# Optimization experiments

Hardware: AMD Instinct MI355X
Metric: run time of the kernel (lower is better)

## Reference

```python
import jax, jax.numpy as jnp
import numpy as np

B, L, E = 4, 2048, 1024
H, DQ, DV = 8, 128, 128
SCALE = 1.0 / np.sqrt(DQ).astype(np.float32)


def setup_inputs() -> dict:
    key = jax.random.key(0)
    ks = jax.random.split(key, 6)
    return {
        "qInputs": jax.random.normal(ks[0], (B, L, E), dtype=jnp.float32),
        "kvInputs": jax.random.normal(ks[1], (B, L, E), dtype=jnp.float32),
        "mask": jnp.zeros((B, H, L, L), dtype=jnp.bool_),
        "W_Q": jax.random.normal(ks[2], (E, H * DQ), dtype=jnp.float32) * 0.02,
        "W_K": jax.random.normal(ks[3], (E, H * DQ), dtype=jnp.float32) * 0.02,
        "W_V": jax.random.normal(ks[4], (E, H * DV), dtype=jnp.float32) * 0.02,
        "W_fc": jax.random.normal(ks[5], (H * DV, E), dtype=jnp.float32) * 0.02,
    }


def reference(qInputs, kvInputs, mask, W_Q, W_K, W_V, W_fc):
    b, lq, _ = qInputs.shape
    lk = kvInputs.shape[1]
    # Projections -> [B, H, L, D]
    Q = (qInputs @ W_Q).reshape(b, lq, H, DQ).transpose(0, 2, 1, 3)
    K = (kvInputs @ W_K).reshape(b, lk, H, DQ).transpose(0, 2, 1, 3)
    V = (kvInputs @ W_V).reshape(b, lk, H, DV).transpose(0, 2, 1, 3)
    # Scaled dot-product with additive mask fill of -1e9
    scores = jnp.einsum("bhqd,bhkd->bhqk", Q, K) * SCALE
    scores = jnp.where(mask, jnp.float32(-1e9), scores)
    attn = jax.nn.softmax(scores, axis=-1)
    ctx = jnp.einsum("bhqk,bhkd->bhqd", attn, V)
    ctx = ctx.transpose(0, 2, 1, 3).reshape(b, lq, H * DV)
    return ctx @ W_fc
```

## Files before the change

### kernel.cpp

```cpp
#include <hip/hip_runtime.h>
#include <stdint.h>

#define LQ 2048
#define EDIM 1024
#define HN 8
#define DH 128
#define BATCH 4
#define SCALE_LOG2E 0.12753785051263942f

typedef short bf16x8 __attribute__((ext_vector_type(8)));
typedef float f32x4 __attribute__((ext_vector_type(4)));
typedef unsigned short u16;
typedef unsigned short u16x4 __attribute__((ext_vector_type(4)));

__device__ __forceinline__ u16 f2bf(float f) {
  union { float f; uint32_t u; } c; c.f = f;
  uint32_t u = c.u;
  return (u16)((u + 0x7fffu + ((u >> 16) & 1u)) >> 16);
}

__device__ __forceinline__ void async16(const void* g, void* l) {
  __builtin_amdgcn_global_load_lds((const __attribute__((address_space(1))) void*)g,
                                   (__attribute__((address_space(3))) void*)l, 16, 0, 0);
}

__device__ __forceinline__ uint32_t lds_b(const u16* p) {
  return (uint32_t)(uintptr_t)(__attribute__((address_space(3))) const u16*)p;
}
__device__ __forceinline__ void ldsr4(bf16x8& d0, bf16x8& d1, bf16x8& d2, bf16x8& d3,
                                      uint32_t a0, uint32_t a1, uint32_t a2, uint32_t a3) {
  asm volatile("ds_read_b128 %0, %4\n\t"
               "ds_read_b128 %1, %5\n\t"
               "ds_read_b128 %2, %6\n\t"
               "ds_read_b128 %3, %7\n\t"
               "s_waitcnt lgkmcnt(0)"
               : "=&v"(d0), "=&v"(d1), "=&v"(d2), "=&v"(d3)
               : "v"(a0), "v"(a1), "v"(a2), "v"(a3));
}
__device__ __forceinline__ void ldsr2(bf16x8& d0, bf16x8& d1, uint32_t a0, uint32_t a1) {
  asm volatile("ds_read_b128 %0, %2\n\t"
               "ds_read_b128 %1, %3\n\t"
               "s_waitcnt lgkmcnt(0)"
               : "=&v"(d0), "=&v"(d1) : "v"(a0), "v"(a1));
}
__device__ __forceinline__ void ldsw16(uint32_t a, u16 v) {
  asm volatile("ds_write_b16 %0, %1" :: "v"(a), "v"((uint32_t)v));
}
__device__ __forceinline__ void lgkm_drain() {
  asm volatile("s_waitcnt lgkmcnt(0)" ::: "memory");
}

__global__ __launch_bounds__(256) void prep_kernel(const float* __restrict__ qIn, const float* __restrict__ kvIn,
                                                   const float* __restrict__ w0, const float* __restrict__ w1,
                                                   const float* __restrict__ w2, const float* __restrict__ w3,
                                                   const unsigned char* __restrict__ mask,
                                                   u16* __restrict__ oq, u16* __restrict__ okv,
                                                   u16* __restrict__ o0, u16* __restrict__ o1,
                                                   u16* __restrict__ o2, u16* __restrict__ o3,
                                                   unsigned char* __restrict__ flags) {
  __shared__ float tile[32][33];
  __shared__ int wany[4];
  const int bid = blockIdx.x;
  const int t = threadIdx.x;
  if (bid < 16384) {
    const float* in = (bid >= 8192) ? kvIn : qIn;
    u16* out = (bid >= 8192) ? okv : oq;
    size_t i = (size_t)(bid & 8191) * 256 + t;
    float4 v = ((const float4*)in)[i];
    u16x4 o;
    o.x = f2bf(v.x); o.y = f2bf(v.y); o.z = f2bf(v.z); o.w = f2bf(v.w);
    ((u16x4*)out)[i] = o;
  } else if (bid < 20480) {
    const int idx = bid - 16384;
    const int z = idx >> 10;
    const int rem = idx & 1023;
    const float* in; u16* out;
    switch (z) {
      case 0: in = w0; out = o0; break;
      case 1: in = w1; out = o1; break;
      case 2: in = w2; out = o2; break;
      default: in = w3; out = o3; break;
    }
    const int tx = t & 31, ty = t >> 5;
    const int x0 = (rem & 31) * 32;
    const int y0 = (rem >> 5) * 32;
#pragma unroll
    for (int j = 0; j < 32; j += 8)
      tile[ty + j][tx] = in[(size_t)(y0 + ty + j) * EDIM + x0 + tx];
    __syncthreads();
#pragma unroll
    for (int j = 0; j < 32; j += 8)
      out[(size_t)(x0 + ty + j) * EDIM + (y0 + tx)] = f2bf(tile[tx][ty + j]);
  } else {
    const int idx = bid - 20480;
    const int bh = idx >> 8;
    const int tile16 = idx & 255;
    const int qt = tile16 >> 4, kt = tile16 & 15;
    const int r = t >> 1;
    const size_t base = ((size_t)bh * LQ + qt * 128 + r) * LQ + kt * 128 + (t & 1) * 64;
    const uint4* p = (const uint4*)(mask + base);
    uint4 a = p[0], c = p[1], d = p[2], e = p[3];
    uint32_t any = a.x | a.y | a.z | a.w | c.x | c.y | c.z | c.w |
                   d.x | d.y | d.z | d.w | e.x | e.y | e.z | e.w;
    int wa = __any(any != 0);
    if ((t & 63) == 0) wany[t >> 6] = wa;
    __syncthreads();
    if (t == 0)
      flags[(size_t)bh * 256 + tile16] = (unsigned char)(wany[0] | wany[1] | wany[2] | wany[3]);
  }
}

struct GemmCore {
  template <typename EpiF>
  static __device__ __forceinline__ void run(const u16* __restrict__ A, const u16* __restrict__ Bt,
                                             int m0, int n0, u16* As, u16* Bs, EpiF epi) {
    const int tid = threadIdx.x;
    const int l = tid & 63;
    const int w = tid >> 6;
    const int wm = (w >> 1) * 64;
    const int wn = (w & 1) * 64;
    const int fm = l & 15;
    const int q4 = l >> 4;
    const int f7 = fm & 7;
    f32x4 acc[4][4] = {};
    for (int k0 = 0; k0 < EDIM; k0 += 64) {
      __syncthreads();
#pragma unroll
      for (int ii = 0; ii < 4; ++ii) {
        const int rloc = w * 32 + ii * 8 + (l >> 3);
        const int cs = (l & 7) ^ (rloc & 7);
        async16(A + (size_t)(m0 + rloc) * EDIM + k0 + cs * 8, &As[(w * 32 + ii * 8) * 64 + l * 8]);
        async16(Bt + (size_t)(n0 + rloc) * EDIM + k0 + cs * 8, &Bs[(w * 32 + ii * 8) * 64 + l * 8]);
      }
      __syncthreads();
#pragma unroll
      for (int ks = 0; ks < 2; ++ks) {
        const int coff = ((ks * 4 + q4) ^ f7) * 8;
        bf16x8 a[4], b[4];
#pragma unroll
        for (int i = 0; i < 4; ++i) a[i] = *(const bf16x8*)&As[(wm + i * 16 + fm) * 64 + coff];
#pragma unroll
        for (int j = 0; j < 4; ++j) b[j] = *(const bf16x8*)&Bs[(wn + j * 16 + fm) * 64 + coff];
#pragma unroll
        for (int i = 0; i < 4; ++i)
#pragma unroll
          for (int j = 0; j < 4; ++j)
            acc[i][j] = __builtin_amdgcn_mfma_f32_16x16x32_bf16(a[i], b[j], acc[i][j], 0, 0, 0);
      }
    }
    const int rr = q4 * 4;
#pragma unroll
    for (int i = 0; i < 4; ++i)
#pragma unroll
      for (int j = 0; j < 4; ++j)
#pragma unroll
        for (int r = 0; r < 4; ++r)
          epi(m0 + wm + i * 16 + rr + r, n0 + wn + j * 16 + fm, acc[i][j][r]);
  }
};

__global__ __launch_bounds__(256) void qkv_gemm(const u16* __restrict__ xq, const u16* __restrict__ xkv,
                                                const u16* __restrict__ WqT, const u16* __restrict__ WkT,
                                                const u16* __restrict__ WvT,
                                                u16* __restrict__ Qb, u16* __restrict__ Kb,
                                                u16* __restrict__ Vt) {
  __shared__ __align__(16) u16 As[128 * 64];
  __shared__ __align__(16) u16 Bs[128 * 64];
  const int z = blockIdx.z;
  if (z == 0) {
    GemmCore::run(xq, WqT, blockIdx.x * 128, blockIdx.y * 128, As, Bs,
                  [&](int gm, int gn, float v) { Qb[(size_t)gm * EDIM + gn] = f2bf(v); });
  } else if (z == 1) {
    GemmCore::run(xkv, WkT, blockIdx.x * 128, blockIdx.y * 128, As, Bs,
                  [&](int gm, int gn, float v) { Kb[(size_t)gm * EDIM + gn] = f2bf(v); });
  } else {
    GemmCore::run(WvT, xkv, blockIdx.y * 128, blockIdx.x * 128, As, Bs,
                  [&](int gm, int gn, float v) {
                    Vt[((size_t)(gn >> 11) * 1024 + gm) * 2048 + (gn & 2047)] = f2bf(v);
                  });
  }
}

__global__ __launch_bounds__(256) void out_gemm(const u16* __restrict__ ctx, const u16* __restrict__ WfcT,
                                                float* __restrict__ out) {
  __shared__ __align__(16) u16 As[128 * 64];
  __shared__ __align__(16) u16 Bs[128 * 64];
  GemmCore::run(ctx, WfcT, blockIdx.x * 128, blockIdx.y * 128, As, Bs,
                [&](int gm, int gn, float v) { out[(size_t)gm * EDIM + gn] = v; });
}

__global__ __launch_bounds__(256, 2) void attn_kernel(const u16* __restrict__ Qb, const u16* __restrict__ Kb,
                                                      const u16* __restrict__ Vt,
                                                      const unsigned char* __restrict__ mask,
                                                      const unsigned char* __restrict__ flags,
                                                      u16* __restrict__ ctx) {
  __shared__ __align__(16) u16 Ktile[2][64 * 128];
  __shared__ __align__(16) u16 Vtile[2][128 * 64];
  __shared__ __align__(16) u16 P[4 * 32 * 64];
  const int tid = threadIdx.x;
  const int l = tid & 63;
  const int w = tid >> 6;
  const int qt = blockIdx.x;
  const int h = blockIdx.y;
  const int b = blockIdx.z;
  const int fm = l & 15;
  const int q4 = l >> 4;
  const int fk = q4 * 8;
  const int f7 = fm & 7;
  const int qbase = qt * 128 + w * 32;
  const int bh = b * HN + h;
  u16* Pw = &P[w * 2048];

  const u16* Kbh = Kb + (size_t)b * LQ * EDIM + h * DH;
  const u16* Vth = Vt + (size_t)bh * DH * LQ;
  const size_t mbase = (size_t)bh * (size_t)LQ * LQ;

  const unsigned char* tf = flags + (size_t)bh * 256 + qt * 16;
  uint32_t fmask = 0;
#pragma unroll
  for (int i = 0; i < 16; ++i) fmask |= (tf[i] ? 1u : 0u) << i;

  bf16x8 qf[2][4];
#pragma unroll
  for (int mt = 0; mt < 2; ++mt)
#pragma unroll
    for (int ks = 0; ks < 4; ++ks)
      qf[mt][ks] = *(const bf16x8*)(Qb + (size_t)(b * LQ + qbase + mt * 16 + fm) * EDIM + h * DH + ks * 32 + fk);

  auto stageK = [&](int kt_, int buf) {
#pragma unroll
    for (int ii = 0; ii < 4; ++ii) {
      const int i = w * 4 + ii;
      const int row = i * 4 + (l >> 4);
      const int g = (l & 15) ^ (row & 7);
      async16(Kbh + (size_t)(kt_ * 64 + row) * EDIM + g * 8, &Ktile[buf][i * 512 + l * 8]);
    }
  };
  auto stageV = [&](int kt_, int buf) {
#pragma unroll
    for (int ii = 0; ii < 4; ++ii) {
      const int i = w * 4 + ii;
      const int row = i * 8 + (l >> 3);
      const int g = (l & 7) ^ (row & 7);
      async16(Vth + (size_t)row * LQ + kt_ * 64 + g * 8, &Vtile[buf][i * 512 + l * 8]);
    }
  };

  stageK(0, 0);
  stageV(0, 0);

  f32x4 o[2][8] = {};
  float lsum[2][4] = {};

  for (int kt = 0; kt < 32; ++kt) {
    const int cur = kt & 1;
    __syncthreads();
    if (kt + 1 < 32) { stageK(kt + 1, 1 - cur); stageV(kt + 1, 1 - cur); }

    const u16* KT = &Ktile[cur][0];
    const u16* VT = &Vtile[cur][0];

    f32x4 s[2][4] = {};
#pragma unroll
    for (int ks = 0; ks < 4; ++ks) {
      const int slot = (ks * 4 + q4) ^ f7;
      bf16x8 kf0, kf1, kf2, kf3;
      ldsr4(kf0, kf1, kf2, kf3,
            lds_b(KT + (0 * 16 + fm) * 128 + slot * 8),
            lds_b(KT + (1 * 16 + fm) * 128 + slot * 8),
            lds_b(KT + (2 * 16 + fm) * 128 + slot * 8),
            lds_b(KT + (3 * 16 + fm) * 128 + slot * 8));
#pragma unroll
      for (int mt = 0; mt < 2; ++mt) {
        s[mt][0] = __builtin_amdgcn_mfma_f32_16x16x32_bf16(qf[mt][ks], kf0, s[mt][0], 0, 0, 0);
        s[mt][1] = __builtin_amdgcn_mfma_f32_16x16x32_bf16(qf[mt][ks], kf1, s[mt][1], 0, 0, 0);
        s[mt][2] = __builtin_amdgcn_mfma_f32_16x16x32_bf16(qf[mt][ks], kf2, s[mt][2], 0, 0, 0);
        s[mt][3] = __builtin_amdgcn_mfma_f32_16x16x32_bf16(qf[mt][ks], kf3, s[mt][3], 0, 0, 0);
      }
    }

    const int hasMask = (fmask >> (kt >> 1)) & 1;
#pragma unroll
    for (int mt = 0; mt < 2; ++mt)
#pragma unroll
      for (int r = 0; r < 4; ++r) {
        float sum = 0.f;
        if (hasMask) {
          const int qr = qbase + mt * 16 + q4 * 4 + r;
          const unsigned char* mrow = mask + mbase + (size_t)qr * LQ + kt * 64 + fm;
#pragma unroll
          for (int nt = 0; nt < 4; ++nt) {
            float e = mrow[nt * 16] ? 0.f : exp2f(s[mt][nt][r] * SCALE_LOG2E);
            s[mt][nt][r] = e;
            sum += e;
          }
        } else {
#pragma unroll
          for (int nt = 0; nt < 4; ++nt) {
            float e = exp2f(s[mt][nt][r] * SCALE_LOG2E);
            s[mt][nt][r] = e;
            sum += e;
          }
        }
#pragma unroll
        for (int off = 1; off < 16; off <<= 1) sum += __shfl_xor(sum, off);
        lsum[mt][r] += sum;
      }

#pragma unroll
    for (int mt = 0; mt < 2; ++mt)
#pragma unroll
      for (int r = 0; r < 4; ++r) {
        const int ql = mt * 16 + q4 * 4 + r;
#pragma unroll
        for (int nt = 0; nt < 4; ++nt) {
          const int chunk = 2 * nt + (fm >> 3);
          const int slot = chunk ^ (ql & 7);
          ldsw16(lds_b(Pw + ql * 64 + slot * 8 + (fm & 7)), f2bf(s[mt][nt][r]));
        }
      }
    lgkm_drain();

#pragma unroll
    for (int ns = 0; ns < 2; ++ns) {
      const int pslot = (4 * ns + q4) ^ f7;
      bf16x8 pf0, pf1;
      ldsr2(pf0, pf1, lds_b(Pw + fm * 64 + pslot * 8), lds_b(Pw + (16 + fm) * 64 + pslot * 8));
      const int vslot = (4 * ns + q4) ^ f7;
      bf16x8 v0, v1, v2, v3, v4, v5, v6, v7;
      ldsr4(v0, v1, v2, v3,
            lds_b(VT + (0 * 16 + fm) * 64 + vslot * 8), lds_b(VT + (1 * 16 + fm) * 64 + vslot * 8),
            lds_b(VT + (2 * 16 + fm) * 64 + vslot * 8), lds_b(VT + (3 * 16 + fm) * 64 + vslot * 8));
      ldsr4(v4, v5, v6, v7,
            lds_b(VT + (4 * 16 + fm) * 64 + vslot * 8), lds_b(VT + (5 * 16 + fm) * 64 + vslot * 8),
            lds_b(VT + (6 * 16 + fm) * 64 + vslot * 8), lds_b(VT + (7 * 16 + fm) * 64 + vslot * 8));
      o[0][0] = __builtin_amdgcn_mfma_f32_16x16x32_bf16(pf0, v0, o[0][0], 0, 0, 0);
      o[1][0] = __builtin_amdgcn_mfma_f32_16x16x32_bf16(pf1, v0, o[1][0], 0, 0, 0);
      o[0][1] = __builtin_amdgcn_mfma_f32_16x16x32_bf16(pf0, v1, o[0][1], 0, 0, 0);
      o[1][1] = __builtin_amdgcn_mfma_f32_16x16x32_bf16(pf1, v1, o[1][1], 0, 0, 0);
      o[0][2] = __builtin_amdgcn_mfma_f32_16x16x32_bf16(pf0, v2, o[0][2], 0, 0, 0);
      o[1][2] = __builtin_amdgcn_mfma_f32_16x16x32_bf16(pf1, v2, o[1][2], 0, 0, 0);
      o[0][3] = __builtin_amdgcn_mfma_f32_16x16x32_bf16(pf0, v3, o[0][3], 0, 0, 0);
      o[1][3] = __builtin_amdgcn_mfma_f32_16x16x32_bf16(pf1, v3, o[1][3], 0, 0, 0);
      o[0][4] = __builtin_amdgcn_mfma_f32_16x16x32_bf16(pf0, v4, o[0][4], 0, 0, 0);
      o[1][4] = __builtin_amdgcn_mfma_f32_16x16x32_bf16(pf1, v4, o[1][4], 0, 0, 0);
      o[0][5] = __builtin_amdgcn_mfma_f32_16x16x32_bf16(pf0, v5, o[0][5], 0, 0, 0);
      o[1][5] = __builtin_amdgcn_mfma_f32_16x16x32_bf16(pf1, v5, o[1][5], 0, 0, 0);
      o[0][6] = __builtin_amdgcn_mfma_f32_16x16x32_bf16(pf0, v6, o[0][6], 0, 0, 0);
      o[1][6] = __builtin_amdgcn_mfma_f32_16x16x32_bf16(pf1, v6, o[1][6], 0, 0, 0);
      o[0][7] = __builtin_amdgcn_mfma_f32_16x16x32_bf16(pf0, v7, o[0][7], 0, 0, 0);
      o[1][7] = __builtin_amdgcn_mfma_f32_16x16x32_bf16(pf1, v7, o[1][7], 0, 0, 0);
    }
  }

#pragma unroll
  for (int mt = 0; mt < 2; ++mt)
#pragma unroll
    for (int r = 0; r < 4; ++r) {
      float inv = 1.f / lsum[mt][r];
      int gq = b * LQ + qbase + mt * 16 + q4 * 4 + r;
#pragma unroll
      for (int dt = 0; dt < 8; ++dt)
        ctx[(size_t)gq * EDIM + h * DH + dt * 16 + fm] = f2bf(o[mt][dt][r] * inv);
    }
}

extern "C" void kernel_launch(void* const* d_in, const int* in_sizes, int n_in,
                              void* d_out, int out_size, void* d_ws, size_t ws_size,
                              hipStream_t stream) {
  const float* qIn = (const float*)d_in[0];
  const float* kvIn = (const float*)d_in[1];
  const unsigned char* mask = (const unsigned char*)d_in[2];
  const float* W_Q = (const float*)d_in[3];
  const float* W_K = (const float*)d_in[4];
  const float* W_V = (const float*)d_in[5];
  const float* W_fc = (const float*)d_in[6];
  float* out = (float*)d_out;

  uint8_t* ws = (uint8_t*)d_ws;
  const size_t MB = 1u << 20;
  u16* xq   = (u16*)(ws);
  u16* xkv  = (u16*)(ws + 16 * MB);
  u16* WqT  = (u16*)(ws + 32 * MB);
  u16* WkT  = (u16*)(ws + 34 * MB);
  u16* WvT  = (u16*)(ws + 36 * MB);
  u16* WfcT = (u16*)(ws + 38 * MB);
  u16* Qb   = (u16*)(ws + 40 * MB);
  u16* Kb   = (u16*)(ws + 56 * MB);
  u16* Vt   = (u16*)(ws + 72 * MB);
  u16* ctx  = (u16*)(ws + 88 * MB);
  unsigned char* flags = (unsigned char*)(ws + 104 * MB);

  prep_kernel<<<28672, 256, 0, stream>>>(qIn, kvIn, W_Q, W_K, W_V, W_fc, mask,
                                         xq, xkv, WqT, WkT, WvT, WfcT, flags);
  qkv_gemm<<<dim3(64, 8, 3), 256, 0, stream>>>(xq, xkv, WqT, WkT, WvT, Qb, Kb, Vt);
  attn_kernel<<<dim3(16, 8, 4), 256, 0, stream>>>(Qb, Kb, Vt, mask, flags, ctx);
  out_gemm<<<dim3(64, 8), 256, 0, stream>>>(ctx, WfcT, out);
}
```

Baseline: 880.6 us.

## Keep softmax probabilities in registers via bpermute and overlap mask scan with QKV GEMM

The attention kernel now computes S transposed (K as the A operand), packs the probabilities to bf16 with v_cvt_pk_bf16_f32, and rearranges them across lanes with ds_bpermute. This removes the per-wave LDS P buffer along with its b16 writes and reads. Row sums are kept per lane and broadcast with a shuffle at the end. Separately, the mask-flag scan moves out of the prep kernel into a fourth z-slice of the QKV GEMM launch, so it can run alongside the GEMM blocks. The cost is extra permute instructions and a more intricate lane mapping.

```diff
diff --git a/kernel.cpp b/kernel.cpp
--- a/kernel.cpp
+++ b/kernel.cpp
@@ -37,29 +37,36 @@
                : "=&v"(d0), "=&v"(d1), "=&v"(d2), "=&v"(d3)
                : "v"(a0), "v"(a1), "v"(a2), "v"(a3));
 }
-__device__ __forceinline__ void ldsr2(bf16x8& d0, bf16x8& d1, uint32_t a0, uint32_t a1) {
-  asm volatile("ds_read_b128 %0, %2\n\t"
-               "ds_read_b128 %1, %3\n\t"
+__device__ __forceinline__ uint32_t cvtpk(float lo, float hi) {
+  uint32_t r;
+  asm("v_cvt_pk_bf16_f32 %0, %1, %2" : "=v"(r) : "v"(lo), "v"(hi));
+  return r;
+}
+__device__ __forceinline__ void bperm8(uint32_t& d0, uint32_t& d1, uint32_t& d2, uint32_t& d3,
+                                       uint32_t& d4, uint32_t& d5, uint32_t& d6, uint32_t& d7,
+                                       uint32_t al, uint32_t ah,
+                                       uint32_t s0, uint32_t s1, uint32_t s2, uint32_t s3) {
+  asm volatile("ds_bpermute_b32 %0, %8, %10\n\t"
+               "ds_bpermute_b32 %1, %8, %11\n\t"
+               "ds_bpermute_b32 %2, %9, %10\n\t"
+               "ds_bpermute_b32 %3, %9, %11\n\t"
+               "ds_bpermute_b32 %4, %8, %12\n\t"
+               "ds_bpermute_b32 %5, %8, %13\n\t"
+               "ds_bpermute_b32 %6, %9, %12\n\t"
+               "ds_bpermute_b32 %7, %9, %13\n\t"
                "s_waitcnt lgkmcnt(0)"
-               : "=&v"(d0), "=&v"(d1) : "v"(a0), "v"(a1));
-}
-__device__ __forceinline__ void ldsw16(uint32_t a, u16 v) {
-  asm volatile("ds_write_b16 %0, %1" :: "v"(a), "v"((uint32_t)v));
-}
-__device__ __forceinline__ void lgkm_drain() {
-  asm volatile("s_waitcnt lgkmcnt(0)" ::: "memory");
+               : "=&v"(d0), "=&v"(d1), "=&v"(d2), "=&v"(d3),
+                 "=&v"(d4), "=&v"(d5), "=&v"(d6), "=&v"(d7)
+               : "v"(al), "v"(ah), "v"(s0), "v"(s1), "v"(s2), "v"(s3));
 }
 
 __global__ __launch_bounds__(256) void prep_kernel(const float* __restrict__ qIn, const float* __restrict__ kvIn,
                                                    const float* __restrict__ w0, const float* __restrict__ w1,
                                                    const float* __restrict__ w2, const float* __restrict__ w3,
-                                                   const unsigned char* __restrict__ mask,
                                                    u16* __restrict__ oq, u16* __restrict__ okv,
                                                    u16* __restrict__ o0, u16* __restrict__ o1,
-                                                   u16* __restrict__ o2, u16* __restrict__ o3,
-                                                   unsigned char* __restrict__ flags) {
+                                                   u16* __restrict__ o2, u16* __restrict__ o3) {
   __shared__ float tile[32][33];
-  __shared__ int wany[4];
   const int bid = blockIdx.x;
   const int t = threadIdx.x;
   if (bid < 16384) {
@@ -70,7 +77,7 @@
     u16x4 o;
     o.x = f2bf(v.x); o.y = f2bf(v.y); o.z = f2bf(v.z); o.w = f2bf(v.w);
     ((u16x4*)out)[i] = o;
-  } else if (bid < 20480) {
+  } else {
     const int idx = bid - 16384;
     const int z = idx >> 10;
     const int rem = idx & 1023;
@@ -91,22 +98,6 @@
 #pragma unroll
     for (int j = 0; j < 32; j += 8)
       out[(size_t)(x0 + ty + j) * EDIM + (y0 + tx)] = f2bf(tile[tx][ty + j]);
-  } else {
-    const int idx = bid - 20480;
-    const int bh = idx >> 8;
-    const int tile16 = idx & 255;
-    const int qt = tile16 >> 4, kt = tile16 & 15;
-    const int r = t >> 1;
-    const size_t base = ((size_t)bh * LQ + qt * 128 + r) * LQ + kt * 128 + (t & 1) * 64;
-    const uint4* p = (const uint4*)(mask + base);
-    uint4 a = p[0], c = p[1], d = p[2], e = p[3];
-    uint32_t any = a.x | a.y | a.z | a.w | c.x | c.y | c.z | c.w |
-                   d.x | d.y | d.z | d.w | e.x | e.y | e.z | e.w;
-    int wa = __any(any != 0);
-    if ((t & 63) == 0) wany[t >> 6] = wa;
-    __syncthreads();
-    if (t == 0)
-      flags[(size_t)bh * 256 + tile16] = (unsigned char)(wany[0] | wany[1] | wany[2] | wany[3]);
   }
 }
 
@@ -163,10 +154,37 @@
                                                 const u16* __restrict__ WqT, const u16* __restrict__ WkT,
                                                 const u16* __restrict__ WvT,
                                                 u16* __restrict__ Qb, u16* __restrict__ Kb,
-                                                u16* __restrict__ Vt) {
+                                                u16* __restrict__ Vt,
+                                                const unsigned char* __restrict__ mask,
+                                                unsigned char* __restrict__ flags) {
   __shared__ __align__(16) u16 As[128 * 64];
   __shared__ __align__(16) u16 Bs[128 * 64];
+  __shared__ int wany[4];
   const int z = blockIdx.z;
+  if (z == 3) {
+    const int t = threadIdx.x;
+    const int unit0 = (blockIdx.x * 8 + blockIdx.y) * 16;
+#pragma unroll 1
+    for (int u = 0; u < 16; ++u) {
+      const int idx = unit0 + u;
+      const int bh = idx >> 8;
+      const int tile16 = idx & 255;
+      const int qt = tile16 >> 4, kt = tile16 & 15;
+      const int r = t >> 1;
+      const size_t base = ((size_t)bh * LQ + qt * 128 + r) * LQ + kt * 128 + (t & 1) * 64;
+      const uint4* p = (const uint4*)(mask + base);
+      uint4 a = p[0], c = p[1], d = p[2], e = p[3];
+      uint32_t any = a.x | a.y | a.z | a.w | c.x | c.y | c.z | c.w |
+                     d.x | d.y | d.z | d.w | e.x | e.y | e.z | e.w;
+      int wa = __any(any != 0);
+      if ((t & 63) == 0) wany[t >> 6] = wa;
+      __syncthreads();
+      if (t == 0)
+        flags[(size_t)bh * 256 + tile16] = (unsigned char)(wany[0] | wany[1] | wany[2] | wany[3]);
+      __syncthreads();
+    }
+    return;
+  }
   if (z == 0) {
     GemmCore::run(xq, WqT, blockIdx.x * 128, blockIdx.y * 128, As, Bs,
                   [&](int gm, int gn, float v) { Qb[(size_t)gm * EDIM + gn] = f2bf(v); });
@@ -196,7 +214,6 @@
                                                       u16* __restrict__ ctx) {
   __shared__ __align__(16) u16 Ktile[2][64 * 128];
   __shared__ __align__(16) u16 Vtile[2][128 * 64];
-  __shared__ __align__(16) u16 P[4 * 32 * 64];
   const int tid = threadIdx.x;
   const int l = tid & 63;
   const int w = tid >> 6;
@@ -209,7 +226,6 @@
   const int f7 = fm & 7;
   const int qbase = qt * 128 + w * 32;
   const int bh = b * HN + h;
-  u16* Pw = &P[w * 2048];
 
   const u16* Kbh = Kb + (size_t)b * LQ * EDIM + h * DH;
   const u16* Vth = Vt + (size_t)bh * DH * LQ;
@@ -250,17 +266,20 @@
   stageV(0, 0);
 
   f32x4 o[2][8] = {};
-  float lsum[2][4] = {};
-
-  for (int kt = 0; kt < 32; ++kt) {
-    const int cur = kt & 1;
+  float lsumv[2] = {0.f, 0.f};
+  const uint32_t al = (uint32_t)((fm + 16 * (2 * (q4 & 1))) << 2);
+  const uint32_t ah = al + 64u;
+  const bool sel_hi = (q4 >> 1) != 0;
+
+  for (int it = 0; it < 32; ++it) {
+    const int cur = it & 1;
     __syncthreads();
-    if (kt + 1 < 32) { stageK(kt + 1, 1 - cur); stageV(kt + 1, 1 - cur); }
+    if (it + 1 < 32) { stageK(it + 1, 1 - cur); stageV(it + 1, 1 - cur); }
 
     const u16* KT = &Ktile[cur][0];
     const u16* VT = &Vtile[cur][0];
 
-    f32x4 s[2][4] = {};
+    f32x4 st[4][2] = {};
 #pragma unroll
     for (int ks = 0; ks < 4; ++ks) {
       const int slot = (ks * 4 + q4) ^ f7;
@@ -272,60 +291,66 @@
             lds_b(KT + (3 * 16 + fm) * 128 + slot * 8));
 #pragma unroll
       for (int mt = 0; mt < 2; ++mt) {
-        s[mt][0] = __builtin_amdgcn_mfma_f32_16x16x32_bf16(qf[mt][ks], kf0, s[mt][0], 0, 0, 0);
-        s[mt][1] = __builtin_amdgcn_mfma_f32_16x16x32_bf16(qf[mt][ks], kf1, s[mt][1], 0, 0, 0);
-        s[mt][2] = __builtin_amdgcn_mfma_f32_16x16x32_bf16(qf[mt][ks], kf2, s[mt][2], 0, 0, 0);
-        s[mt][3] = __builtin_amdgcn_mfma_f32_16x16x32_bf16(qf[mt][ks], kf3, s[mt][3], 0, 0, 0);
-      }
-    }
-
-    const int hasMask = (fmask >> (kt >> 1)) & 1;
-#pragma unroll
-    for (int mt = 0; mt < 2; ++mt)
-#pragma unroll
-      for (int r = 0; r < 4; ++r) {
-        float sum = 0.f;
-        if (hasMask) {
-          const int qr = qbase + mt * 16 + q4 * 4 + r;
-          const unsigned char* mrow = mask + mbase + (size_t)qr * LQ + kt * 64 + fm;
-#pragma unroll
-          for (int nt = 0; nt < 4; ++nt) {
-            float e = mrow[nt * 16] ? 0.f : exp2f(s[mt][nt][r] * SCALE_LOG2E);
-            s[mt][nt][r] = e;
-            sum += e;
-          }
-        } else {
-#pragma unroll
-          for (int nt = 0; nt < 4; ++nt) {
-            float e = exp2f(s[mt][nt][r] * SCALE_LOG2E);
-            s[mt][nt][r] = e;
+        st[0][mt] = __builtin_amdgcn_mfma_f32_16x16x32_bf16(kf0, qf[mt][ks], st[0][mt], 0, 0, 0);
+        st[1][mt] = __builtin_amdgcn_mfma_f32_16x16x32_bf16(kf1, qf[mt][ks], st[1][mt], 0, 0, 0);
+        st[2][mt] = __builtin_amdgcn_mfma_f32_16x16x32_bf16(kf2, qf[mt][ks], st[2][mt], 0, 0, 0);
+        st[3][mt] = __builtin_amdgcn_mfma_f32_16x16x32_bf16(kf3, qf[mt][ks], st[3][mt], 0, 0, 0);
+      }
+    }
+
+    const int hasMask = (fmask >> (it >> 1)) & 1;
+    uint32_t pk[2][4][2];
+#pragma unroll
+    for (int mt = 0; mt < 2; ++mt) {
+      float sum = 0.f;
+      if (hasMask) {
+        const unsigned char* mrow = mask + mbase + (size_t)(qbase + mt * 16 + fm) * LQ + it * 64 + q4 * 4;
+#pragma unroll
+        for (int kt = 0; kt < 4; ++kt) {
+          const uint32_t mv = *(const uint32_t*)(mrow + kt * 16);
+#pragma unroll
+          for (int r = 0; r < 4; ++r) {
+            float e = ((mv >> (8 * r)) & 0xffu) ? 0.f : exp2f(st[kt][mt][r] * SCALE_LOG2E);
+            st[kt][mt][r] = e;
             sum += e;
           }
         }
-#pragma unroll
-        for (int off = 1; off < 16; off <<= 1) sum += __shfl_xor(sum, off);
-        lsum[mt][r] += sum;
-      }
-
-#pragma unroll
-    for (int mt = 0; mt < 2; ++mt)
-#pragma unroll
-      for (int r = 0; r < 4; ++r) {
-        const int ql = mt * 16 + q4 * 4 + r;
-#pragma unroll
-        for (int nt = 0; nt < 4; ++nt) {
-          const int chunk = 2 * nt + (fm >> 3);
-          const int slot = chunk ^ (ql & 7);
-          ldsw16(lds_b(Pw + ql * 64 + slot * 8 + (fm & 7)), f2bf(s[mt][nt][r]));
-        }
-      }
-    lgkm_drain();
+      } else {
+#pragma unroll
+        for (int kt = 0; kt < 4; ++kt)
+#pragma unroll
+          for (int r = 0; r < 4; ++r) {
+            float e = exp2f(st[kt][mt][r] * SCALE_LOG2E);
+            st[kt][mt][r] = e;
+            sum += e;
+          }
+      }
+      sum += __shfl_xor(sum, 16);
+      sum += __shfl_xor(sum, 32);
+      lsumv[mt] += sum;
+#pragma unroll
+      for (int kt = 0; kt < 4; ++kt) {
+        pk[mt][kt][0] = cvtpk(st[kt][mt][0], st[kt][mt][1]);
+        pk[mt][kt][1] = cvtpk(st[kt][mt][2], st[kt][mt][3]);
+      }
+    }
 
 #pragma unroll
     for (int ns = 0; ns < 2; ++ns) {
-      const int pslot = (4 * ns + q4) ^ f7;
-      bf16x8 pf0, pf1;
-      ldsr2(pf0, pf1, lds_b(Pw + fm * 64 + pslot * 8), lds_b(Pw + (16 + fm) * 64 + pslot * 8));
+      bf16x8 paf[2];
+#pragma unroll
+      for (int mt = 0; mt < 2; ++mt) {
+        uint32_t t0, t1, t2, t3, u0, u1, u2, u3;
+        bperm8(t0, t1, t2, t3, u0, u1, u2, u3, al, ah,
+               pk[mt][2 * ns][0], pk[mt][2 * ns][1],
+               pk[mt][2 * ns + 1][0], pk[mt][2 * ns + 1][1]);
+        union { uint32_t u[4]; bf16x8 v; } fb;
+        fb.u[0] = sel_hi ? u0 : t0;
+        fb.u[1] = sel_hi ? u1 : t1;
+        fb.u[2] = sel_hi ? u2 : t2;
+        fb.u[3] = sel_hi ? u3 : t3;
+        paf[mt] = fb.v;
+      }
       const int vslot = (4 * ns + q4) ^ f7;
       bf16x8 v0, v1, v2, v3, v4, v5, v6, v7;
       ldsr4(v0, v1, v2, v3,
@@ -334,22 +359,22 @@
       ldsr4(v4, v5, v6, v7,
             lds_b(VT + (4 * 16 + fm) * 64 + vslot * 8), lds_b(VT + (5 * 16 + fm) * 64 + vslot * 8),
             lds_b(VT + (6 * 16 + fm) * 64 + vslot * 8), lds_b(VT + (7 * 16 + fm) * 64 + vslot * 8));
-      o[0][0] = __builtin_amdgcn_mfma_f32_16x16x32_bf16(pf0, v0, o[0][0], 0, 0, 0);
-      o[1][0] = __builtin_amdgcn_mfma_f32_16x16x32_bf16(pf1, v0, o[1][0], 0, 0, 0);
-      o[0][1] = __builtin_amdgcn_mfma_f32_16x16x32_bf16(pf0, v1, o[0][1], 0, 0, 0);
-      o[1][1] = __builtin_amdgcn_mfma_f32_16x16x32_bf16(pf1, v1, o[1][1], 0, 0, 0);
-      o[0][2] = __builtin_amdgcn_mfma_f32_16x16x32_bf16(pf0, v2, o[0][2], 0, 0, 0);
-      o[1][2] = __builtin_amdgcn_mfma_f32_16x16x32_bf16(pf1, v2, o[1][2], 0, 0, 0);
-      o[0][3] = __builtin_amdgcn_mfma_f32_16x16x32_bf16(pf0, v3, o[0][3], 0, 0, 0);
-      o[1][3] = __builtin_amdgcn_mfma_f32_16x16x32_bf16(pf1, v3, o[1][3], 0, 0, 0);
-      o[0][4] = __builtin_amdgcn_mfma_f32_16x16x32_bf16(pf0, v4, o[0][4], 0, 0, 0);
-      o[1][4] = __builtin_amdgcn_mfma_f32_16x16x32_bf16(pf1, v4, o[1][4], 0, 0, 0);
-      o[0][5] = __builtin_amdgcn_mfma_f32_16x16x32_bf16(pf0, v5, o[0][5], 0, 0, 0);
-      o[1][5] = __builtin_amdgcn_mfma_f32_16x16x32_bf16(pf1, v5, o[1][5], 0, 0, 0);
-      o[0][6] = __builtin_amdgcn_mfma_f32_16x16x32_bf16(pf0, v6, o[0][6], 0, 0, 0);
-      o[1][6] = __builtin_amdgcn_mfma_f32_16x16x32_bf16(pf1, v6, o[1][6], 0, 0, 0);
-      o[0][7] = __builtin_amdgcn_mfma_f32_16x16x32_bf16(pf0, v7, o[0][7], 0, 0, 0);
-      o[1][7] = __builtin_amdgcn_mfma_f32_16x16x32_bf16(pf1, v7, o[1][7], 0, 0, 0);
+      o[0][0] = __builtin_amdgcn_mfma_f32_16x16x32_bf16(paf[0], v0, o[0][0], 0, 0, 0);
+      o[1][0] = __builtin_amdgcn_mfma_f32_16x16x32_bf16(paf[1], v0, o[1][0], 0, 0, 0);
+      o[0][1] = __builtin_amdgcn_mfma_f32_16x16x32_bf16(paf[0], v1, o[0][1], 0, 0, 0);
+      o[1][1] = __builtin_amdgcn_mfma_f32_16x16x32_bf16(paf[1], v1, o[1][1], 0, 0, 0);
+      o[0][2] = __builtin_amdgcn_mfma_f32_16x16x32_bf16(paf[0], v2, o[0][2], 0, 0, 0);
+      o[1][2] = __builtin_amdgcn_mfma_f32_16x16x32_bf16(paf[1], v2, o[1][2], 0, 0, 0);
+      o[0][3] = __builtin_amdgcn_mfma_f32_16x16x32_bf16(paf[0], v3, o[0][3], 0, 0, 0);
+      o[1][3] = __builtin_amdgcn_mfma_f32_16x16x32_bf16(paf[1], v3, o[1][3], 0, 0, 0);
+      o[0][4] = __builtin_amdgcn_mfma_f32_16x16x32_bf16(paf[0], v4, o[0][4], 0, 0, 0);
+      o[1][4] = __builtin_amdgcn_mfma_f32_16x16x32_bf16(paf[1], v4, o[1][4], 0, 0, 0);
+      o[0][5] = __builtin_amdgcn_mfma_f32_16x16x32_bf16(paf[0], v5, o[0][5], 0, 0, 0);
+      o[1][5] = __builtin_amdgcn_mfma_f32_16x16x32_bf16(paf[1], v5, o[1][5], 0, 0, 0);
+      o[0][6] = __builtin_amdgcn_mfma_f32_16x16x32_bf16(paf[0], v6, o[0][6], 0, 0, 0);
+      o[1][6] = __builtin_amdgcn_mfma_f32_16x16x32_bf16(paf[1], v6, o[1][6], 0, 0, 0);
+      o[0][7] = __builtin_amdgcn_mfma_f32_16x16x32_bf16(paf[0], v7, o[0][7], 0, 0, 0);
+      o[1][7] = __builtin_amdgcn_mfma_f32_16x16x32_bf16(paf[1], v7, o[1][7], 0, 0, 0);
     }
   }
 
@@ -357,7 +382,7 @@
   for (int mt = 0; mt < 2; ++mt)
 #pragma unroll
     for (int r = 0; r < 4; ++r) {
-      float inv = 1.f / lsum[mt][r];
+      float inv = 1.f / __shfl(lsumv[mt], q4 * 4 + r);
       int gq = b * LQ + qbase + mt * 16 + q4 * 4 + r;
 #pragma unroll
       for (int dt = 0; dt < 8; ++dt)
@@ -391,9 +416,9 @@
   u16* ctx  = (u16*)(ws + 88 * MB);
   unsigned char* flags = (unsigned char*)(ws + 104 * MB);
 
-  prep_kernel<<<28672, 256, 0, stream>>>(qIn, kvIn, W_Q, W_K, W_V, W_fc, mask,
-                                         xq, xkv, WqT, WkT, WvT, WfcT, flags);
-  qkv_gemm<<<dim3(64, 8, 3), 256, 0, stream>>>(xq, xkv, WqT, WkT, WvT, Qb, Kb, Vt);
+  prep_kernel<<<20480, 256, 0, stream>>>(qIn, kvIn, W_Q, W_K, W_V, W_fc,
+                                         xq, xkv, WqT, WkT, WvT, WfcT);
+  qkv_gemm<<<dim3(64, 8, 4), 256, 0, stream>>>(xq, xkv, WqT, WkT, WvT, Qb, Kb, Vt, mask, flags);
   attn_kernel<<<dim3(16, 8, 4), 256, 0, stream>>>(Qb, Kb, Vt, mask, flags, ctx);
   out_gemm<<<dim3(64, 8), 256, 0, stream>>>(ctx, WfcT, out);
 }
```

New measurement: 846.6 us. 3.9% less time.
